# Kernel optimization log

Measured on AMD Instinct MI355X. Metric: run time of the kernel, lower is better.

The kernel has to match this reference:

```python
import jax, jax.numpy as jnp
import numpy as np

N_NODES = 50000
N_EDGES = 400000
DIMS = [512, 512, 512, 512]  # input + 3 hidden
NUM_CLASSES = 40


def setup_inputs() -> dict:
    key = jax.random.key(0)
    ks = jax.random.split(key, 16)
    feat = jax.random.normal(ks[0], (N_NODES, DIMS[0]), dtype=jnp.float32)
    src = jax.random.randint(ks[1], (N_EDGES,), 0, N_NODES, dtype=jnp.int32)
    dst = jax.random.randint(ks[2], (N_EDGES,), 0, N_NODES, dtype=jnp.int32)
    params = {}
    for i in range(3):
        fan_in = DIMS[i]
        s = 1.0 / np.sqrt(fan_in)
        params[f"W{i}"] = jax.random.uniform(ks[3 + 2 * i], (DIMS[i], DIMS[i + 1]), jnp.float32, -s, s)
        params[f"b{i}"] = jax.random.uniform(ks[4 + 2 * i], (DIMS[i + 1],), jnp.float32, -s, s)
    s = 1.0 / np.sqrt(DIMS[-1])
    params["Wc"] = jax.random.uniform(ks[10], (DIMS[-1], NUM_CLASSES), jnp.float32, -s, s)
    params["bc"] = jax.random.uniform(ks[11], (NUM_CLASSES,), jnp.float32, -s, s)
    return {"feat": feat, "src": src, "dst": dst, **params}


def _gin_layer(h, src, dst, W, b):
    # DGL GINConv, aggregator='sum', eps=0: rst = (1+eps)*h + sum_{j in N(i)} h_j
    agg = jax.ops.segment_sum(h[src], dst, num_segments=N_NODES)  # [N, D]
    return jax.nn.relu((h + agg) @ W + b)  # apply_func Linear, then relu (dropout p=0)


def reference(feat, src, dst, W0, b0, W1, b1, W2, b2, Wc, bc):
    h = _gin_layer(feat, src, dst, W0, b0)
    h = _gin_layer(h, src, dst, W1, b1)
    h = _gin_layer(h, src, dst, W2, b2)
    return h @ Wc + bc  # [N, num_classes]
```

## Files before the change

### kernel.cpp

```cpp
#include <hip/hip_runtime.h>

#define N_NODES 50000
#define N_EDGES 400000
#define D 512
#define NCLS 40
#define SCAN_BLOCKS ((N_NODES + 255) / 256)
#define CSTRIDE 260
#define SLOT 12288

typedef __attribute__((ext_vector_type(8))) __bf16 bf16x8;
typedef __attribute__((ext_vector_type(4))) float f32x4;
typedef __attribute__((ext_vector_type(4))) float float4v;
typedef __attribute__((ext_vector_type(8))) unsigned short ushort8v;
typedef __attribute__((ext_vector_type(4))) unsigned short ushort4v;

#define AS1 __attribute__((address_space(1)))
#define AS3 __attribute__((address_space(3)))

__device__ __forceinline__ float bf2f(unsigned short u) {
  union { unsigned int i; float f; } v; v.i = ((unsigned int)u) << 16; return v.f;
}
__device__ __forceinline__ unsigned short f2bf(float f) {
  union { float f; unsigned int i; } v; v.f = f;
  unsigned int u = v.i;
  u += 0x7fffu + ((u >> 16) & 1u);
  return (unsigned short)(u >> 16);
}

__global__ void hist_kernel(const int* __restrict__ dst, int* __restrict__ counts) {
  int e = blockIdx.x * blockDim.x + threadIdx.x;
  if (e < N_EDGES) atomicAdd(&counts[dst[e]], 1);
}

__global__ __launch_bounds__(256) void scan_local_kernel(const int* __restrict__ counts,
    int* __restrict__ incl, int* __restrict__ bsum) {
  __shared__ int s[256];
  int i = blockIdx.x * 256 + threadIdx.x;
  int v = (i < N_NODES) ? counts[i] : 0;
  s[threadIdx.x] = v;
  __syncthreads();
#pragma unroll
  for (int o = 1; o < 256; o <<= 1) {
    int t = (threadIdx.x >= o) ? s[threadIdx.x - o] : 0;
    __syncthreads();
    s[threadIdx.x] += t;
    __syncthreads();
  }
  if (i < N_NODES) incl[i] = s[threadIdx.x];
  if (threadIdx.x == 255) bsum[blockIdx.x] = s[255];
}

__global__ __launch_bounds__(256) void scan_bsum_kernel(int* __restrict__ bsum) {
  __shared__ int s[256];
  int v = (threadIdx.x < SCAN_BLOCKS) ? bsum[threadIdx.x] : 0;
  s[threadIdx.x] = v;
  __syncthreads();
#pragma unroll
  for (int o = 1; o < 256; o <<= 1) {
    int t = (threadIdx.x >= o) ? s[threadIdx.x - o] : 0;
    __syncthreads();
    s[threadIdx.x] += t;
    __syncthreads();
  }
  if (threadIdx.x < SCAN_BLOCKS) bsum[threadIdx.x] = s[threadIdx.x] - v;
}

__global__ __launch_bounds__(256) void scan_finish_kernel(const int* __restrict__ counts,
    const int* __restrict__ bsum, int* __restrict__ row_ptr, int* __restrict__ cursor) {
  int i = blockIdx.x * 256 + threadIdx.x;
  if (i < N_NODES) {
    int inc = cursor[i] + bsum[blockIdx.x];
    row_ptr[i + 1] = inc;
    cursor[i] = inc - counts[i];
    if (i == 0) row_ptr[0] = 0;
  }
}

__global__ void fill_kernel(const int* __restrict__ src, const int* __restrict__ dst,
                            int* __restrict__ cursor, int* __restrict__ esrc) {
  int e = blockIdx.x * blockDim.x + threadIdx.x;
  if (e < N_EDGES) {
    int pos = atomicAdd(&cursor[dst[e]], 1);
    esrc[pos] = src[e];
  }
}

__global__ void cvt_feat_kernel(const float* __restrict__ feat, unsigned short* __restrict__ hb) {
  size_t i = (size_t)(blockIdx.x * blockDim.x + threadIdx.x) * 4;
  if (i < (size_t)N_NODES * D) {
    float4v v = *(const float4v*)&feat[i];
    ushort4v o;
    o[0] = f2bf(v[0]); o[1] = f2bf(v[1]); o[2] = f2bf(v[2]); o[3] = f2bf(v[3]);
    *(ushort4v*)&hb[i] = o;
  }
}

__global__ void cvt_w_all_kernel(const float* __restrict__ W0, const float* __restrict__ W1,
                                 const float* __restrict__ W2, const float* __restrict__ Wc,
                                 unsigned short* __restrict__ Wt, unsigned short* __restrict__ Wct) {
  int i = blockIdx.x * blockDim.x + threadIdx.x;
  if (i < 3 * D * D) {
    int l = i >> 18;
    int r = i & (D * D - 1);
    int n = r >> 9, k = r & 511;
    const float* W = (l == 0) ? W0 : ((l == 1) ? W1 : W2);
    Wt[i] = f2bf(W[k * D + n]);
  } else {
    int r = i - 3 * D * D;
    if (r < 48 * D) {
      int n = r >> 9, k = r & 511;
      Wct[r] = (n < NCLS) ? f2bf(Wc[k * NCLS + n]) : (unsigned short)0;
    }
  }
}

__global__ __launch_bounds__(256) void agg_kernel(const unsigned short* __restrict__ hb,
    const int* __restrict__ row_ptr, const int* __restrict__ esrc,
    unsigned short* __restrict__ zb) {
  int w = threadIdx.x >> 6, lane = threadIdx.x & 63;
  int node = blockIdx.x * 4 + w;
  int col = lane * 8;
  const unsigned short* hcol = hb + col;
  float acc[8];
  ushort8v v = *(const ushort8v*)&hcol[(size_t)node * D];
#pragma unroll
  for (int t = 0; t < 8; ++t) acc[t] = bf2f(v[t]);
  int s = row_ptr[node], e = row_ptr[node + 1];
  int j = s;
  for (; j + 4 <= e; j += 4) {
    int i0 = esrc[j + 0], i1 = esrc[j + 1], i2 = esrc[j + 2], i3 = esrc[j + 3];
    ushort8v v0 = *(const ushort8v*)&hcol[(size_t)i0 * D];
    ushort8v v1 = *(const ushort8v*)&hcol[(size_t)i1 * D];
    ushort8v v2 = *(const ushort8v*)&hcol[(size_t)i2 * D];
    ushort8v v3 = *(const ushort8v*)&hcol[(size_t)i3 * D];
#pragma unroll
    for (int t = 0; t < 8; ++t) acc[t] += bf2f(v0[t]);
#pragma unroll
    for (int t = 0; t < 8; ++t) acc[t] += bf2f(v1[t]);
#pragma unroll
    for (int t = 0; t < 8; ++t) acc[t] += bf2f(v2[t]);
#pragma unroll
    for (int t = 0; t < 8; ++t) acc[t] += bf2f(v3[t]);
  }
  for (; j < e; ++j) {
    int sn = esrc[j];
    ushort8v nv = *(const ushort8v*)&hcol[(size_t)sn * D];
#pragma unroll
    for (int t = 0; t < 8; ++t) acc[t] += bf2f(nv[t]);
  }
  ushort8v o;
#pragma unroll
  for (int t = 0; t < 8; ++t) o[t] = f2bf(acc[t]);
  *(ushort8v*)&zb[(size_t)node * D + col] = o;
}

__global__ __launch_bounds__(512, 4) void gemm_kernel(
    const unsigned short* __restrict__ Z, const unsigned short* __restrict__ Wt,
    const float* __restrict__ bias, unsigned short* __restrict__ Hout, int M) {
  __shared__ unsigned short smem[3 * SLOT];
  const int tid = threadIdx.x;
  const int lane = tid & 63;
  const int w = tid >> 6;
  const int wm = (w >> 2) * 64;
  const int wn = (w & 3) * 64;
  const int quad = lane >> 4;
  const int r16 = lane & 15;

  const int nwg = gridDim.x * gridDim.y;
  const int lin = blockIdx.y * gridDim.x + blockIdx.x;
  const int q = nwg >> 3, r = nwg & 7;
  const int xcd = lin & 7, idx = lin >> 3;
  const int wg = (xcd < r ? xcd * (q + 1) : r * (q + 1) + (xcd - r) * q) + idx;
  const int n0 = (wg & 1) * 256;
  const int m0 = (wg >> 1) * 128;

  f32x4 acc[4][4];
#pragma unroll
  for (int i = 0; i < 4; ++i)
#pragma unroll
    for (int j = 0; j < 4; ++j)
      acc[i][j] = (f32x4){0.f, 0.f, 0.f, 0.f};

  const int srow = lane >> 2;
  const int skk = (lane & 3) * 8;
  int gm_st = m0 + w * 16 + srow; if (gm_st > M - 1) gm_st = M - 1;
  const unsigned short* Zst = Z + (size_t)gm_st * D + skk;
  const unsigned short* Bst0 = Wt + (size_t)(n0 + w * 32 + srow) * D + skk;
  const unsigned short* Bst1 = Wt + (size_t)(n0 + w * 32 + 16 + srow) * D + skk;

  auto stage = [&](int kt_, unsigned short* p) {
    __builtin_amdgcn_global_load_lds((AS1 void*)(void*)(Zst + kt_ * 32),
                                     (AS3 void*)(p + w * 512), 16, 0, 0);
    __builtin_amdgcn_global_load_lds((AS1 void*)(void*)(Bst0 + kt_ * 32),
                                     (AS3 void*)(p + 4096 + (w * 2 + 0) * 512), 16, 0, 0);
    __builtin_amdgcn_global_load_lds((AS1 void*)(void*)(Bst1 + kt_ * 32),
                                     (AS3 void*)(p + 4096 + (w * 2 + 1) * 512), 16, 0, 0);
  };

  unsigned short* p0 = smem;
  unsigned short* p1 = smem + SLOT;
  unsigned short* p2 = smem + 2 * SLOT;

  stage(0, p0);
  stage(1, p1);

  for (int kt = 0; kt < 16; ++kt) {
    if (kt < 15) asm volatile("s_waitcnt vmcnt(3)" ::: "memory");
    else         asm volatile("s_waitcnt vmcnt(0)" ::: "memory");
    __builtin_amdgcn_s_barrier();
    __builtin_amdgcn_sched_barrier(0);
    if (kt + 2 < 16) stage(kt + 2, p2);
    __builtin_amdgcn_sched_barrier(0);
    const unsigned short* Ac = p0;
    const unsigned short* Bc = p0 + 4096;
    bf16x8 a[4];
#pragma unroll
    for (int i = 0; i < 4; ++i)
      a[i] = *(const bf16x8*)&Ac[(wm + i * 16 + r16) * 32 + quad * 8];
#pragma unroll
    for (int j = 0; j < 4; ++j) {
      bf16x8 b = *(const bf16x8*)&Bc[(wn + j * 16 + r16) * 32 + quad * 8];
#pragma unroll
      for (int i = 0; i < 4; ++i)
        acc[i][j] = __builtin_amdgcn_mfma_f32_16x16x32_bf16(a[i], b, acc[i][j], 0, 0, 0);
    }
    unsigned short* t = p0; p0 = p1; p1 = p2; p2 = t;
  }

  __syncthreads();
  unsigned short* Cs = smem;
#pragma unroll
  for (int j = 0; j < 4; ++j) {
    float bv = bias[n0 + wn + j * 16 + r16];
#pragma unroll
    for (int i = 0; i < 4; ++i) {
      int crow = wm + i * 16 + quad * 4;
      int ccol = wn + j * 16 + r16;
#pragma unroll
      for (int rr = 0; rr < 4; ++rr) {
        float vv = acc[i][j][rr] + bv;
        vv = vv > 0.f ? vv : 0.f;
        Cs[(crow + rr) * CSTRIDE + ccol] = f2bf(vv);
      }
    }
  }
  __syncthreads();
#pragma unroll
  for (int it = 0; it < 8; ++it) {
    int row = it * 16 + (tid >> 5);
    int colofs = (tid & 31) * 8;
    int gm = m0 + row;
    if (gm < M) {
      ushort8v vv = *(const ushort8v*)&Cs[row * CSTRIDE + colofs];
      *(ushort8v*)&Hout[(size_t)gm * D + n0 + colofs] = vv;
    }
  }
}

__global__ __launch_bounds__(256) void cls_kernel(const unsigned short* __restrict__ hb,
    const unsigned short* __restrict__ Wct, const float* __restrict__ bc,
    float* __restrict__ out) {
  int w = threadIdx.x >> 6, lane = threadIdx.x & 63;
  int quad = lane >> 4, r16 = lane & 15;
  int nb = blockIdx.x * 64 + w * 16;
  int arow = nb + r16; if (arow > N_NODES - 1) arow = N_NODES - 1;
  f32x4 acc[3];
#pragma unroll
  for (int j = 0; j < 3; ++j) acc[j] = (f32x4){0.f, 0.f, 0.f, 0.f};
#pragma unroll 4
  for (int kt = 0; kt < 16; ++kt) {
    int kk = kt * 32 + quad * 8;
    bf16x8 a = *(const bf16x8*)&hb[(size_t)arow * D + kk];
#pragma unroll
    for (int j = 0; j < 3; ++j) {
      bf16x8 b = *(const bf16x8*)&Wct[(size_t)(j * 16 + r16) * D + kk];
      acc[j] = __builtin_amdgcn_mfma_f32_16x16x32_bf16(a, b, acc[j], 0, 0, 0);
    }
  }
#pragma unroll
  for (int j = 0; j < 3; ++j) {
    int gn = j * 16 + r16;
    if (gn < NCLS) {
      float bv = bc[gn];
#pragma unroll
      for (int r = 0; r < 4; ++r) {
        int gm = nb + quad * 4 + r;
        if (gm < N_NODES) out[(size_t)gm * NCLS + gn] = acc[j][r] + bv;
      }
    }
  }
}

extern "C" void kernel_launch(void* const* d_in, const int* in_sizes, int n_in,
                              void* d_out, int out_size, void* d_ws, size_t ws_size,
                              hipStream_t stream) {
  const float* feat = (const float*)d_in[0];
  const int* src = (const int*)d_in[1];
  const int* dst = (const int*)d_in[2];
  const float* W0 = (const float*)d_in[3];
  const float* b0 = (const float*)d_in[4];
  const float* W1 = (const float*)d_in[5];
  const float* b1 = (const float*)d_in[6];
  const float* W2 = (const float*)d_in[7];
  const float* b2 = (const float*)d_in[8];
  const float* Wc = (const float*)d_in[9];
  const float* bc = (const float*)d_in[10];
  float* out = (float*)d_out;

  char* ws = (char*)d_ws;
  size_t off = 0;
  auto alloc = [&](size_t bytes) {
    char* p = ws + off;
    off += (bytes + 255) & ~(size_t)255;
    return p;
  };
  unsigned short* hb = (unsigned short*)alloc((size_t)N_NODES * D * 2);
  unsigned short* zb = (unsigned short*)alloc((size_t)N_NODES * D * 2);
  unsigned short* Wt = (unsigned short*)alloc((size_t)3 * D * D * 2);
  unsigned short* Wct = (unsigned short*)alloc((size_t)48 * D * 2);
  int* row_ptr = (int*)alloc((size_t)(N_NODES + 1) * 4);
  int* counts  = (int*)alloc((size_t)N_NODES * 4);
  int* cursor  = (int*)alloc((size_t)N_NODES * 4);
  int* esrc    = (int*)alloc((size_t)N_EDGES * 4);
  int* bsum    = (int*)alloc((size_t)256 * 4);

  hipMemsetAsync(counts, 0, (size_t)N_NODES * 4, stream);
  hist_kernel<<<(N_EDGES + 255) / 256, 256, 0, stream>>>(dst, counts);
  scan_local_kernel<<<SCAN_BLOCKS, 256, 0, stream>>>(counts, cursor, bsum);
  scan_bsum_kernel<<<1, 256, 0, stream>>>(bsum);
  scan_finish_kernel<<<SCAN_BLOCKS, 256, 0, stream>>>(counts, bsum, row_ptr, cursor);
  fill_kernel<<<(N_EDGES + 255) / 256, 256, 0, stream>>>(src, dst, cursor, esrc);

  cvt_feat_kernel<<<(N_NODES * D / 4 + 255) / 256, 256, 0, stream>>>(feat, hb);
  cvt_w_all_kernel<<<(3 * D * D + 48 * D + 255) / 256, 256, 0, stream>>>(W0, W1, W2, Wc, Wt, Wct);

  dim3 ggrid(2, (N_NODES + 127) / 128);
  const float* bs[3] = {b0, b1, b2};
  for (int l = 0; l < 3; ++l) {
    agg_kernel<<<N_NODES / 4, 256, 0, stream>>>(hb, row_ptr, esrc, zb);
    gemm_kernel<<<ggrid, 512, 0, stream>>>(zb, Wt + (size_t)l * D * D, bs[l], hb, N_NODES);
  }
  cls_kernel<<<(N_NODES + 63) / 64, 256, 0, stream>>>(hb, Wct, bc, out);
}
```

Measured before the change: 579.1 us.

## Fuse CSR build and conversion kernels into one cooperative kernel

```diff
diff --git a/kernel.cpp b/kernel.cpp
--- a/kernel.cpp
+++ b/kernel.cpp
@@ -1,4 +1,7 @@
 #include <hip/hip_runtime.h>
+#include <hip/hip_cooperative_groups.h>
+
+namespace cg = cooperative_groups;
 
 #define N_NODES 50000
 #define N_EDGES 400000
@@ -27,90 +30,91 @@
   return (unsigned short)(u >> 16);
 }
 
-__global__ void hist_kernel(const int* __restrict__ dst, int* __restrict__ counts) {
-  int e = blockIdx.x * blockDim.x + threadIdx.x;
-  if (e < N_EDGES) atomicAdd(&counts[dst[e]], 1);
-}
-
-__global__ __launch_bounds__(256) void scan_local_kernel(const int* __restrict__ counts,
-    int* __restrict__ incl, int* __restrict__ bsum) {
+__global__ __launch_bounds__(256, 4) void build_all_kernel(
+    const float* __restrict__ feat, const float* __restrict__ W0,
+    const float* __restrict__ W1, const float* __restrict__ W2,
+    const float* __restrict__ Wc, const int* __restrict__ src,
+    const int* __restrict__ dst, unsigned short* __restrict__ hb,
+    unsigned short* __restrict__ Wt, unsigned short* __restrict__ Wct,
+    int* __restrict__ row_ptr, int* __restrict__ counts,
+    int* __restrict__ cursor, int* __restrict__ esrc, int* __restrict__ bsum) {
+  cg::grid_group grid = cg::this_grid();
+  const int T = gridDim.x * blockDim.x;
+  const int gtid = blockIdx.x * blockDim.x + threadIdx.x;
   __shared__ int s[256];
-  int i = blockIdx.x * 256 + threadIdx.x;
-  int v = (i < N_NODES) ? counts[i] : 0;
-  s[threadIdx.x] = v;
-  __syncthreads();
-#pragma unroll
-  for (int o = 1; o < 256; o <<= 1) {
-    int t = (threadIdx.x >= o) ? s[threadIdx.x - o] : 0;
-    __syncthreads();
-    s[threadIdx.x] += t;
-    __syncthreads();
-  }
-  if (i < N_NODES) incl[i] = s[threadIdx.x];
-  if (threadIdx.x == 255) bsum[blockIdx.x] = s[255];
-}
-
-__global__ __launch_bounds__(256) void scan_bsum_kernel(int* __restrict__ bsum) {
-  __shared__ int s[256];
-  int v = (threadIdx.x < SCAN_BLOCKS) ? bsum[threadIdx.x] : 0;
-  s[threadIdx.x] = v;
-  __syncthreads();
-#pragma unroll
-  for (int o = 1; o < 256; o <<= 1) {
-    int t = (threadIdx.x >= o) ? s[threadIdx.x - o] : 0;
-    __syncthreads();
-    s[threadIdx.x] += t;
-    __syncthreads();
-  }
-  if (threadIdx.x < SCAN_BLOCKS) bsum[threadIdx.x] = s[threadIdx.x] - v;
-}
-
-__global__ __launch_bounds__(256) void scan_finish_kernel(const int* __restrict__ counts,
-    const int* __restrict__ bsum, int* __restrict__ row_ptr, int* __restrict__ cursor) {
-  int i = blockIdx.x * 256 + threadIdx.x;
-  if (i < N_NODES) {
-    int inc = cursor[i] + bsum[blockIdx.x];
-    row_ptr[i + 1] = inc;
-    cursor[i] = inc - counts[i];
-    if (i == 0) row_ptr[0] = 0;
-  }
-}
-
-__global__ void fill_kernel(const int* __restrict__ src, const int* __restrict__ dst,
-                            int* __restrict__ cursor, int* __restrict__ esrc) {
-  int e = blockIdx.x * blockDim.x + threadIdx.x;
-  if (e < N_EDGES) {
-    int pos = atomicAdd(&cursor[dst[e]], 1);
-    esrc[pos] = src[e];
-  }
-}
-
-__global__ void cvt_feat_kernel(const float* __restrict__ feat, unsigned short* __restrict__ hb) {
-  size_t i = (size_t)(blockIdx.x * blockDim.x + threadIdx.x) * 4;
-  if (i < (size_t)N_NODES * D) {
+
+  for (int i = gtid; i < N_NODES; i += T) counts[i] = 0;
+  for (size_t c = gtid; c < (size_t)N_NODES * D / 4; c += (size_t)T) {
+    size_t i = c * 4;
     float4v v = *(const float4v*)&feat[i];
     ushort4v o;
     o[0] = f2bf(v[0]); o[1] = f2bf(v[1]); o[2] = f2bf(v[2]); o[3] = f2bf(v[3]);
     *(ushort4v*)&hb[i] = o;
   }
-}
-
-__global__ void cvt_w_all_kernel(const float* __restrict__ W0, const float* __restrict__ W1,
-                                 const float* __restrict__ W2, const float* __restrict__ Wc,
-                                 unsigned short* __restrict__ Wt, unsigned short* __restrict__ Wct) {
-  int i = blockIdx.x * blockDim.x + threadIdx.x;
-  if (i < 3 * D * D) {
-    int l = i >> 18;
-    int r = i & (D * D - 1);
-    int n = r >> 9, k = r & 511;
-    const float* W = (l == 0) ? W0 : ((l == 1) ? W1 : W2);
-    Wt[i] = f2bf(W[k * D + n]);
-  } else {
-    int r = i - 3 * D * D;
-    if (r < 48 * D) {
+  for (int i = gtid; i < 3 * D * D + 48 * D; i += T) {
+    if (i < 3 * D * D) {
+      int l = i >> 18;
+      int r = i & (D * D - 1);
+      int n = r >> 9, k = r & 511;
+      const float* W = (l == 0) ? W0 : ((l == 1) ? W1 : W2);
+      Wt[i] = f2bf(W[k * D + n]);
+    } else {
+      int r = i - 3 * D * D;
       int n = r >> 9, k = r & 511;
       Wct[r] = (n < NCLS) ? f2bf(Wc[k * NCLS + n]) : (unsigned short)0;
     }
+  }
+  grid.sync();
+
+  for (int e = gtid; e < N_EDGES; e += T) atomicAdd(&counts[dst[e]], 1);
+  grid.sync();
+
+  if (blockIdx.x < SCAN_BLOCKS) {
+    int i = blockIdx.x * 256 + threadIdx.x;
+    int v = (i < N_NODES) ? counts[i] : 0;
+    s[threadIdx.x] = v;
+    __syncthreads();
+#pragma unroll
+    for (int o = 1; o < 256; o <<= 1) {
+      int t = (threadIdx.x >= o) ? s[threadIdx.x - o] : 0;
+      __syncthreads();
+      s[threadIdx.x] += t;
+      __syncthreads();
+    }
+    if (i < N_NODES) cursor[i] = s[threadIdx.x];
+    if (threadIdx.x == 255) bsum[blockIdx.x] = s[255];
+  }
+  grid.sync();
+
+  if (blockIdx.x == 0) {
+    int v = (threadIdx.x < SCAN_BLOCKS) ? bsum[threadIdx.x] : 0;
+    s[threadIdx.x] = v;
+    __syncthreads();
+#pragma unroll
+    for (int o = 1; o < 256; o <<= 1) {
+      int t = (threadIdx.x >= o) ? s[threadIdx.x - o] : 0;
+      __syncthreads();
+      s[threadIdx.x] += t;
+      __syncthreads();
+    }
+    if (threadIdx.x < SCAN_BLOCKS) bsum[threadIdx.x] = s[threadIdx.x] - v;
+  }
+  grid.sync();
+
+  if (blockIdx.x < SCAN_BLOCKS) {
+    int i = blockIdx.x * 256 + threadIdx.x;
+    if (i < N_NODES) {
+      int inc = cursor[i] + bsum[blockIdx.x];
+      row_ptr[i + 1] = inc;
+      cursor[i] = inc - counts[i];
+      if (i == 0) row_ptr[0] = 0;
+    }
+  }
+  grid.sync();
+
+  for (int e = gtid; e < N_EDGES; e += T) {
+    int pos = atomicAdd(&cursor[dst[e]], 1);
+    esrc[pos] = src[e];
   }
 }
 
@@ -324,15 +328,12 @@
   int* esrc    = (int*)alloc((size_t)N_EDGES * 4);
   int* bsum    = (int*)alloc((size_t)256 * 4);
 
-  hipMemsetAsync(counts, 0, (size_t)N_NODES * 4, stream);
-  hist_kernel<<<(N_EDGES + 255) / 256, 256, 0, stream>>>(dst, counts);
-  scan_local_kernel<<<SCAN_BLOCKS, 256, 0, stream>>>(counts, cursor, bsum);
-  scan_bsum_kernel<<<1, 256, 0, stream>>>(bsum);
-  scan_finish_kernel<<<SCAN_BLOCKS, 256, 0, stream>>>(counts, bsum, row_ptr, cursor);
-  fill_kernel<<<(N_EDGES + 255) / 256, 256, 0, stream>>>(src, dst, cursor, esrc);
-
-  cvt_feat_kernel<<<(N_NODES * D / 4 + 255) / 256, 256, 0, stream>>>(feat, hb);
-  cvt_w_all_kernel<<<(3 * D * D + 48 * D + 255) / 256, 256, 0, stream>>>(W0, W1, W2, Wc, Wt, Wct);
+  void* kargs[] = {(void*)&feat, (void*)&W0, (void*)&W1, (void*)&W2, (void*)&Wc,
+                   (void*)&src, (void*)&dst, (void*)&hb, (void*)&Wt, (void*)&Wct,
+                   (void*)&row_ptr, (void*)&counts, (void*)&cursor, (void*)&esrc,
+                   (void*)&bsum};
+  hipLaunchCooperativeKernel((const void*)build_all_kernel, dim3(1024), dim3(256),
+                             kargs, 0, stream);
 
   dim3 ggrid(2, (N_NODES + 127) / 128);
   const float* bs[3] = {b0, b1, b2};
```

Measured after the change: 1.100 ms. 89.9% more time.
